# Kernel optimization log

Measured on AMD Instinct MI355X. Metric: run time of the kernel, lower is better.

Reference implementation:

```python
import jax, jax.numpy as jnp
import numpy as np

N, M, KNN, KUP, POS_DIM = 15872, 35637, 5, 20, 32


def _pos_emb_table(n, d):
    # transformer-style sinusoidal table (matches PosEmb._define_pos_emb)
    pos = np.arange(n, dtype=np.float32)[:, None]
    i2 = np.arange(0, d, 2, dtype=np.float32)
    div = 10000.0 ** (i2 / d)
    pe = np.zeros((n, d), dtype=np.float32)
    pe[:, 0::2] = np.sin(pos / div)
    pe[:, 1::2] = np.cos(pos / div)
    return jnp.asarray(pe)


def _lrelu(x):
    return jnp.where(x > 0, x, 0.2 * x)


def _gather(x, idx):
    # x: [B,n,d], idx: [B,m,k] -> [B,m,k,d]
    return jax.vmap(lambda xb, ib: xb[ib])(x, idx)


def _knn_idx(x, k):
    # x: [B,n,d]; k nearest excluding self (torch knn drops column 0 of topk)
    xx = jnp.sum(x * x, axis=-1)
    neg = 2.0 * jnp.einsum('bnd,bmd->bnm', x, x) - xx[:, :, None] - xx[:, None, :]
    _, idx = jax.lax.top_k(neg, k + 1)
    return idx[..., 1:]


def _emb_block(feat, idx, ec_w1, ec_s1, ec_h1, ec_w2, ec_b2,
               w1, s1, h1, w2, s2, h2, w3, s3, h3, w4, b4):
    # get_graph_feature: [B,n,k,2*in] = cat(nbr - ctr, ctr)
    nbr = _gather(feat, idx)
    ctr = jnp.broadcast_to(feat[:, :, None, :], nbr.shape)
    e = jnp.concatenate([nbr - ctr, ctr], axis=-1)
    # edge_conv (1x1 conv2d = per-edge linear); BN folded into scale/shift (eval mode)
    e = _lrelu(jnp.einsum('bnkc,oc->bnko', e, ec_w1) * ec_s1 + ec_h1)
    e = jnp.einsum('bnkc,oc->bnko', e, ec_w2) + ec_b2
    f1 = jnp.max(e, axis=2)                                   # max over k neighbors -> [B,n,out]
    fmax = jnp.broadcast_to(jnp.max(f1, axis=1, keepdims=True), f1.shape)
    favg = jnp.broadcast_to(jnp.mean(f1, axis=1, keepdims=True), f1.shape)
    h = jnp.concatenate([feat, f1, fmax, favg], axis=-1)      # [B,n,3*out+in]
    # fc_out: 1x1 conv1d stack = per-point MLP with folded BN + LeakyReLU
    h = _lrelu(h @ w1.T * s1 + h1)
    h = _lrelu(h @ w2.T * s2 + h2)
    h = _lrelu(h @ w3.T * s3 + h3)
    return h @ w4.T + b4


def _forward(lx, ldx, pos_emb,
             b0_ec_w1, b0_ec_s1, b0_ec_h1, b0_ec_w2, b0_ec_b2,
             b0_fc_w1, b0_fc_s1, b0_fc_h1, b0_fc_w2, b0_fc_s2, b0_fc_h2,
             b0_fc_w3, b0_fc_s3, b0_fc_h3, b0_fc_w4, b0_fc_b4,
             b1_ec_w1, b1_ec_s1, b1_ec_h1, b1_ec_w2, b1_ec_b2,
             b1_fc_w1, b1_fc_s1, b1_fc_h1, b1_fc_w2, b1_fc_s2, b1_fc_h2,
             b1_fc_w3, b1_fc_s3, b1_fc_h3, b1_fc_w4, b1_fc_b4,
             up_inputs, up_w0, up_s0, up_h0, up_w_rest, up_s_rest, up_h_rest, up_wf, up_bf,
             dec_w0, dec_b0, dec_w1, dec_b1, dec_w2, dec_b2, dec_w3, dec_b3,
             dec_w4, dec_b4, dec_wf, dec_bf,
             idx0, up_idx):
    B = ldx.shape[0]
    feat_in = jnp.concatenate([ldx, jnp.broadcast_to(pos_emb[None], (B,) + pos_emb.shape)], axis=-1)  # [B,N,35]
    f0 = _emb_block(feat_in, idx0,
                    b0_ec_w1, b0_ec_s1, b0_ec_h1, b0_ec_w2, b0_ec_b2,
                    b0_fc_w1, b0_fc_s1, b0_fc_h1, b0_fc_w2, b0_fc_s2, b0_fc_h2,
                    b0_fc_w3, b0_fc_s3, b0_fc_h3, b0_fc_w4, b0_fc_b4)   # [B,N,64]
    idx1 = _knn_idx(f0, KNN)                                            # dynamic feature-space KNN
    f1 = _emb_block(f0, idx1,
                    b1_ec_w1, b1_ec_s1, b1_ec_h1, b1_ec_w2, b1_ec_b2,
                    b1_fc_w1, b1_fc_s1, b1_fc_h1, b1_fc_w2, b1_fc_s2, b1_fc_h2,
                    b1_fc_w3, b1_fc_s3, b1_fc_h3, b1_fc_w4, b1_fc_b4)   # [B,N,128]
    x_feat = jnp.concatenate([feat_in, f0, f1], axis=-1)                # [B,N,227]
    # Upscale: SIREN-activated 1x1-conv stack -> softmax interpolation weights over KUP lo-res nbrs
    h = jnp.sin(jnp.einsum('bmkc,oc->bmko', up_inputs[:B], up_w0) * up_s0 + up_h0)
    for i in range(up_w_rest.shape[0]):
        h = jnp.sin(jnp.einsum('bmkc,oc->bmko', h, up_w_rest[i]) * up_s_rest[i] + up_h_rest[i])
    logits = jnp.einsum('bmkc,oc->bmko', h, up_wf) + up_bf              # [B,M,KUP,1]
    w = jax.nn.softmax(logits, axis=2)
    grouped = _gather(x_feat, up_idx)                                   # [B,M,KUP,227]
    z = jnp.sum(w * grouped, axis=2)                                    # [B,M,227]
    # SIREN decoder: dims [227,256,128,64,32,16,3]; zip with 5 mods applies first 5 layers + head
    h = jnp.sin(30.0 * (z @ dec_w0.T + dec_b0))
    h = jnp.sin(h @ dec_w1.T + dec_b1)
    h = jnp.sin(h @ dec_w2.T + dec_b2)
    h = jnp.sin(h @ dec_w3.T + dec_b3)
    h = jnp.sin(h @ dec_w4.T + dec_b4)
    return h @ dec_wf.T + dec_bf                                        # [B,M,3]


def setup_inputs():
    key = jax.random.key(0)
    ks = iter(jax.random.split(key, 100))
    def rn(*s):
        return jax.random.normal(next(ks), s, jnp.float32) * 0.05
    def sc(*s):
        return jax.random.uniform(next(ks), s, jnp.float32, minval=0.5, maxval=1.5)
    inp = {}
    inp['lx'] = jax.random.normal(next(ks), (1, N, 3), jnp.float32)
    inp['ldx'] = jax.random.normal(next(ks), (1, N, 3), jnp.float32)
    inp['pos_emb'] = _pos_emb_table(N, POS_DIM)
    inp['idx0'] = jax.random.randint(next(ks), (1, N, KNN), 0, N - 1)
    # EmbModule 0: in=35, out=64
    inp['b0_ec_w1'], inp['b0_ec_s1'], inp['b0_ec_h1'] = rn(128, 70), sc(128), rn(128)
    inp['b0_ec_w2'], inp['b0_ec_b2'] = rn(64, 128), rn(64)
    inp['b0_fc_w1'], inp['b0_fc_s1'], inp['b0_fc_h1'] = rn(192, 227), sc(192), rn(192)
    inp['b0_fc_w2'], inp['b0_fc_s2'], inp['b0_fc_h2'] = rn(128, 192), sc(128), rn(128)
    inp['b0_fc_w3'], inp['b0_fc_s3'], inp['b0_fc_h3'] = rn(64, 128), sc(64), rn(64)
    inp['b0_fc_w4'], inp['b0_fc_b4'] = rn(64, 64), rn(64)
    # EmbModule 1: in=64, out=128
    inp['b1_ec_w1'], inp['b1_ec_s1'], inp['b1_ec_h1'] = rn(256, 128), sc(256), rn(256)
    inp['b1_ec_w2'], inp['b1_ec_b2'] = rn(128, 256), rn(128)
    inp['b1_fc_w1'], inp['b1_fc_s1'], inp['b1_fc_h1'] = rn(384, 448), sc(384), rn(384)
    inp['b1_fc_w2'], inp['b1_fc_s2'], inp['b1_fc_h2'] = rn(256, 384), sc(256), rn(256)
    inp['b1_fc_w3'], inp['b1_fc_s3'], inp['b1_fc_h3'] = rn(128, 256), sc(128), rn(128)
    inp['b1_fc_w4'], inp['b1_fc_b4'] = rn(128, 128), rn(128)
    inp['up_inputs'] = jax.random.uniform(next(ks), (1, M, KUP, 7), jnp.float32)
    inp['up_idx'] = jax.random.randint(next(ks), (1, M, KUP), 0, N - 1)
    inp['up_w0'], inp['up_s0'], inp['up_h0'] = rn(128, 7), sc(128), rn(128)
    inp['up_w_rest'], inp['up_s_rest'], inp['up_h_rest'] = rn(7, 128, 128), sc(7, 128), rn(7, 128)
    inp['up_wf'], inp['up_bf'] = rn(1, 128), rn(1)
    # SIREN decoder
    dd = [227, 256, 128, 64, 32, 16]
    for i in range(5):
        inp['dec_w%d' % i], inp['dec_b%d' % i] = rn(dd[i + 1], dd[i]), rn(dd[i + 1])
    inp['dec_wf'], inp['dec_bf'] = rn(3, 16), rn(3)
    return inp


def reference(lx, ldx, pos_emb, idx0,
              b0_ec_w1, b0_ec_s1, b0_ec_h1, b0_ec_w2, b0_ec_b2,
              b0_fc_w1, b0_fc_s1, b0_fc_h1, b0_fc_w2, b0_fc_s2, b0_fc_h2,
              b0_fc_w3, b0_fc_s3, b0_fc_h3, b0_fc_w4, b0_fc_b4,
              b1_ec_w1, b1_ec_s1, b1_ec_h1, b1_ec_w2, b1_ec_b2,
              b1_fc_w1, b1_fc_s1, b1_fc_h1, b1_fc_w2, b1_fc_s2, b1_fc_h2,
              b1_fc_w3, b1_fc_s3, b1_fc_h3, b1_fc_w4, b1_fc_b4,
              up_inputs, up_idx, up_w0, up_s0, up_h0,
              up_w_rest, up_s_rest, up_h_rest, up_wf, up_bf,
              dec_w0, dec_b0, dec_w1, dec_b1, dec_w2, dec_b2, dec_w3, dec_b3,
              dec_w4, dec_b4, dec_wf, dec_bf):
    return _forward(lx, ldx, pos_emb,
                    b0_ec_w1, b0_ec_s1, b0_ec_h1, b0_ec_w2, b0_ec_b2,
                    b0_fc_w1, b0_fc_s1, b0_fc_h1, b0_fc_w2, b0_fc_s2, b0_fc_h2,
                    b0_fc_w3, b0_fc_s3, b0_fc_h3, b0_fc_w4, b0_fc_b4,
                    b1_ec_w1, b1_ec_s1, b1_ec_h1, b1_ec_w2, b1_ec_b2,
                    b1_fc_w1, b1_fc_s1, b1_fc_h1, b1_fc_w2, b1_fc_s2, b1_fc_h2,
                    b1_fc_w3, b1_fc_s3, b1_fc_h3, b1_fc_w4, b1_fc_b4,
                    up_inputs, up_w0, up_s0, up_h0, up_w_rest, up_s_rest, up_h_rest, up_wf, up_bf,
                    dec_w0, dec_b0, dec_w1, dec_b1, dec_w2, dec_b2, dec_w3, dec_b3,
                    dec_w4, dec_b4, dec_wf, dec_bf,
                    idx0, up_idx)
```

## Files before the change

### kernel.cpp

```cpp
#include <hip/hip_runtime.h>
#include <hip/hip_bf16.h>
#include <math.h>

#define N_PTS 15872
#define M_PTS 35637
#define KNN_K 5
#define KUP   20
#define UP_ROWS (M_PTS * KUP)
#define NTILE (N_PTS/32)
#define N_EDGE (N_PTS*KNN_K)
#define CDIV(a,b) (((a)+(b)-1)/(b))

typedef __hip_bfloat16 bf16;
typedef unsigned int uint;
typedef unsigned short ushort_t;
__device__ __forceinline__ float b2f(bf16 x){ return __bfloat162float(x); }

__device__ __forceinline__ uint f2bf_bits(float x){
  uint u = __float_as_uint(x);
  return (u + 0x7FFFu + ((u>>16)&1u)) >> 16;
}

__device__ __forceinline__ ushort_t f2h_bits(float x){
  union { _Float16 h; ushort_t u; } c; c.h = (_Float16)x; return c.u;
}

typedef __attribute__((ext_vector_type(8))) short bf16x8;
typedef __attribute__((ext_vector_type(8))) _Float16 f16x8;
typedef __attribute__((ext_vector_type(16))) float f32x16;
union FragAB { bf16x8 v; uint u[4]; };
union FragB  { bf16x8 v; uint4 q; };
union FragH  { f16x8 v; uint4 q; _Float16 h[8]; };
union Acc16  { f32x16 v; float f[16]; };

__global__ void flag_k(const uint* __restrict__ pos_raw, int* __restrict__ flag){
  if (threadIdx.x == 0 && blockIdx.x == 0)
    flag[0] = (pos_raw[0] == 0x3F800000u) ? 1 : 0;
}

struct CvtTab { const void* src[52]; int start[52]; };
__global__ __launch_bounds__(256) void cvt_all_k(CvtTab tab, float* __restrict__ dst,
                                                 const int* __restrict__ flag, int total){
  int i = blockIdx.x*256 + threadIdx.x;
  if (i >= total) return;
  int s = 0;
#pragma unroll 1
  for (int k = 1; k < 52; k++) if (tab.start[k] <= i) s = k;
  int off = i - tab.start[s];
  float v = flag[0] ? b2f(((const bf16*)tab.src[s])[off]) : ((const float*)tab.src[s])[off];
  dst[i] = v;
}

__global__ void packfrag16_k(const float* __restrict__ w, const float* __restrict__ sr,
                             ushort_t* __restrict__ out, int n){
  int i = blockIdx.x*256 + threadIdx.x;
  if (i >= n) return;
  int j = i & 7;
  int lam = (i >> 3) & 63;
  int fg = i >> 9;
  int t = fg & 3, ks = (fg >> 2) & 1, Q = (fg >> 3) & 3, l = fg >> 5;
  int nn = t*32 + (lam & 31);
  int kk = Q*32 + ks*16 + (lam >> 5)*8 + j;
  float x = w[l*16384 + nn*128 + kk] * sr[l*128 + nn];
  out[i] = f2h_bits(x);
}

__global__ void packw_mfma_k(const float* __restrict__ w, ushort_t* __restrict__ whi,
                             ushort_t* __restrict__ wlo, int N, int K, int Kpad, int total){
  int i = blockIdx.x*256 + threadIdx.x;
  if (i >= total) return;
  int j = i & 7;
  int lane = (i >> 3) & 63;
  int fr = i >> 9;
  int nq = Kpad >> 5;
  int ks = fr & 1;
  int q  = (fr >> 1) % nq;
  int nt = (fr >> 1) / nq;
  int n = nt*32 + (lane & 31);
  int k = q*32 + ks*16 + (lane >> 5)*8 + j;
  float x = (n < N && k < K) ? w[(size_t)n*K + k] : 0.f;
  uint hb = f2bf_bits(x);
  uint lb = f2bf_bits(x - __uint_as_float(hb << 16));
  whi[i] = (ushort_t)hb;
  wlo[i] = (ushort_t)lb;
}

__global__ void packknn_k(const float* __restrict__ xf, const float* __restrict__ nr,
                          ushort_t* __restrict__ ahi, ushort_t* __restrict__ alo,
                          ushort_t* __restrict__ bhi, ushort_t* __restrict__ blo){
  int i = blockIdx.x*256 + threadIdx.x;
  if (i >= NTILE*5*64*8) return;
  int e = i & 7;
  int lane = (i >> 3) & 63;
  int rest = i >> 9;
  int kc = rest % 5, jt = rest / 5;
  int n = jt*32 + (lane & 31);
  int k = kc*16 + (lane >> 5)*8 + e;
  float f = (k < 64) ? xf[(size_t)n*227 + 35 + k] : 0.f;
  float av, bv;
  if (k < 64)      { av = 2.f*f;   bv = f; }
  else if (k == 64){ av = nr[n];   bv = -1.f; }
  else if (k == 65){ av = 1.f;     bv = -nr[n]; }
  else             { av = 0.f;     bv = 0.f; }
  uint ah = f2bf_bits(av); uint al = f2bf_bits(av - __uint_as_float(ah<<16));
  uint bh = f2bf_bits(bv); uint bl = f2bf_bits(bv - __uint_as_float(bh<<16));
  ahi[i] = (ushort_t)ah; alo[i] = (ushort_t)al;
  bhi[i] = (ushort_t)bh; blo[i] = (ushort_t)bl;
}

__global__ void fillmark_k(bf16* __restrict__ out, int n){
  int i = blockIdx.x*256 + threadIdx.x;
  if (i < n) out[i] = __float2bfloat16(12345.0f);
}

template<int EPI, int ACT>
__global__ __launch_bounds__(256) void gemm_k(
    const float* __restrict__ A, int lda,
    const float* __restrict__ W, int ldw,
    const float* __restrict__ scale, const float* __restrict__ shift,
    float gmul, float* __restrict__ C, int ldc,
    int M, int Nout, int K)
{
  __shared__ __align__(16) float As[16][64];
  __shared__ __align__(16) float Ws[16][64];
  const int tid = threadIdx.x;
  const int tx = tid & 15, ty = tid >> 4;
  const int bm = blockIdx.x * 64, bn = blockIdx.y * 64;
  const int ar = tid >> 2, ak = (tid & 3) * 4;
  float acc[4][4] = {};
  for (int k0 = 0; k0 < K; k0 += 16) {
    float a0=0.f,a1=0.f,a2=0.f,a3=0.f;
    int grow = bm + ar;
    if (grow < M) {
      const float* ap = A + (size_t)grow * lda + (k0 + ak);
      int rem = K - (k0 + ak);
      if (rem >= 4) { a0=ap[0]; a1=ap[1]; a2=ap[2]; a3=ap[3]; }
      else { if(rem>0)a0=ap[0]; if(rem>1)a1=ap[1]; if(rem>2)a2=ap[2]; }
    }
    float w0=0.f,w1=0.f,w2=0.f,w3=0.f;
    int gn = bn + ar;
    if (gn < Nout) {
      const float* wp = W + (size_t)gn * ldw + (k0 + ak);
      int rem = K - (k0 + ak);
      if (rem >= 4) { w0=wp[0]; w1=wp[1]; w2=wp[2]; w3=wp[3]; }
      else { if(rem>0)w0=wp[0]; if(rem>1)w1=wp[1]; if(rem>2)w2=wp[2]; }
    }
    __syncthreads();
    As[ak+0][ar]=a0; As[ak+1][ar]=a1; As[ak+2][ar]=a2; As[ak+3][ar]=a3;
    Ws[ak+0][ar]=w0; Ws[ak+1][ar]=w1; Ws[ak+2][ar]=w2; Ws[ak+3][ar]=w3;
    __syncthreads();
#pragma unroll
    for (int kk = 0; kk < 16; kk++) {
      float4 av = *reinterpret_cast<const float4*>(&As[kk][ty*4]);
      float4 wv = *reinterpret_cast<const float4*>(&Ws[kk][tx*4]);
      float aa[4] = {av.x,av.y,av.z,av.w};
      float ww[4] = {wv.x,wv.y,wv.z,wv.w};
#pragma unroll
      for (int i=0;i<4;i++)
#pragma unroll
        for (int j=0;j<4;j++) acc[i][j] += aa[i]*ww[j];
    }
  }
#pragma unroll
  for (int i=0;i<4;i++){
    int m = bm + ty*4 + i;
    if (m >= M) continue;
#pragma unroll
    for (int j=0;j<4;j++){
      int n = bn + tx*4 + j;
      if (n >= Nout) continue;
      float v = acc[i][j];
      if (EPI==0)      v = v * scale[n] + shift[n];
      else if (EPI==1) v = v + shift[n];
      else             v = (v + shift[n]) * gmul;
      if (ACT==1)      v = v > 0.f ? v : 0.2f*v;
      else if (ACT==2) v = sinf(v);
      C[(size_t)m*ldc + n] = v;
    }
  }
}

struct MLayer { int K, N, Kq, Nt, woff, soff, hoff, epi, act; float gmul; };
struct MCfg { MLayer L[6]; };

template<int NL, int OUTMODE>
__global__ __launch_bounds__(256) void mlp_fused_k(
    const float* __restrict__ A0, int lda0, int K0, int M,
    MCfg cfg,
    const ushort_t* __restrict__ wh, const ushort_t* __restrict__ wl,
    const float* __restrict__ wc,
    float* __restrict__ Cout, int ldc,
    void* __restrict__ oflg, const int* __restrict__ flag)
{
  __shared__ __align__(16) uint slab[64*256];
  const int tid = threadIdx.x;
  const int lane = tid & 63;
  const int wv = tid >> 6;
  const int np = lane & 31;
  const int hb2 = lane >> 5;
  const int rhalf = wv & 1, thalf = wv >> 1;
  const int rb = blockIdx.x * 64;
  const int row_l = rhalf*32 + np;

  for (int e = tid; e < 64*64; e += 256) {
    int r = e >> 6, g = e & 63;
    int gr = rb + r;
    uint p[4];
#pragma unroll
    for (int u=0;u<4;u++){
      int k = g*4+u;
      float f = (gr < M && k < K0) ? A0[(size_t)gr*lda0 + k] : 0.f;
      uint hb = f2bf_bits(f);
      uint lb = f2bf_bits(f - __uint_as_float(hb<<16));
      p[u] = (hb<<16) | lb;
    }
    *(uint4*)&slab[r*256 + (((g ^ r) & 63)<<2)] = make_uint4(p[0],p[1],p[2],p[3]);
  }
  __syncthreads();

#pragma unroll 1
  for (int l = 0; l < NL; l++){
    const int N = cfg.L[l].N, Kq = cfg.L[l].Kq, Nt = cfg.L[l].Nt;
    const int woff = cfg.L[l].woff, soff = cfg.L[l].soff, hoff = cfg.L[l].hoff;
    const int epi = cfg.L[l].epi, actf = cfg.L[l].act;
    const float gmul = cfg.L[l].gmul;
    Acc16 acc[4];
#pragma unroll
    for (int u=0;u<4;u++)
#pragma unroll
      for (int i=0;i<16;i++) acc[u].f[i] = 0.f;

#pragma unroll 1
    for (int q = 0; q < Kq; q++){
#pragma unroll
      for (int ks = 0; ks < 2; ks++){
        int g0 = (q*32 + ks*16 + hb2*8) >> 2;
        uint4 a0 = *(const uint4*)&slab[row_l*256 + ((((g0  ) ^ row_l) & 63)<<2)];
        uint4 a1 = *(const uint4*)&slab[row_l*256 + ((((g0+1) ^ row_l) & 63)<<2)];
        uint au[8] = {a0.x,a0.y,a0.z,a0.w,a1.x,a1.y,a1.z,a1.w};
        FragAB ah, al;
#pragma unroll
        for (int p=0;p<4;p++){
          ah.u[p] = (au[2*p]>>16)     | (au[2*p+1] & 0xFFFF0000u);
          al.u[p] = (au[2*p]&0xFFFFu) | (au[2*p+1]<<16);
        }
#pragma unroll
        for (int u=0;u<4;u++){
          int t = thalf + u*2;
          if (t < Nt){
            size_t fb = (size_t)woff + ((size_t)((t*Kq + q)*2 + ks))*512 + (size_t)lane*8;
            FragB bh, bl;
            bh.q = *(const uint4*)(wh + fb);
            bl.q = *(const uint4*)(wl + fb);
            acc[u].v = __builtin_amdgcn_mfma_f32_32x32x16_bf16(ah.v, bh.v, acc[u].v, 0,0,0);
            acc[u].v = __builtin_amdgcn_mfma_f32_32x32x16_bf16(al.v, bh.v, acc[u].v, 0,0,0);
            acc[u].v = __builtin_amdgcn_mfma_f32_32x32x16_bf16(ah.v, bl.v, acc[u].v, 0,0,0);
          }
        }
      }
    }
    __syncthreads();
#pragma unroll
    for (int u=0;u<4;u++){
      int t = thalf + u*2;
      if (t < Nt){
        int col = t*32 + np;
        if (col < N){
          float scv = (epi==0) ? wc[soff+col] : 0.f;
          float shv = wc[hoff+col];
#pragma unroll
          for (int reg=0;reg<16;reg++){
            int r32 = (reg&3) + 8*(reg>>2) + 4*hb2;
            float v = acc[u].f[reg];
            if (epi==0)      v = v*scv + shv;
            else if (epi==1) v = v + shv;
            else             v = (v + shv)*gmul;
            if (actf==1)      v = v > 0.f ? v : 0.2f*v;
            else if (actf==2) v = __sinf(v);
            if (l == NL-1){
              int gr = rb + rhalf*32 + r32;
              if (gr < M){
                if (OUTMODE==0) Cout[(size_t)gr*ldc + col] = v;
                else {
                  if (!(fabsf(v) < 1e30f)) v = 777.0f;
                  size_t oi = (size_t)gr*3 + col;
                  if (flag[0]) ((bf16*)oflg)[oi] = __float2bfloat16(v);
                  else         ((float*)oflg)[oi] = v;
                }
              }
            } else {
              int r = rhalf*32 + r32;
              uint hb = f2bf_bits(v);
              uint lb = f2bf_bits(v - __uint_as_float(hb<<16));
              slab[r*256 + ((((col>>2) ^ r) & 63)<<2) + (col&3)] = (hb<<16) | lb;
            }
          }
        }
      }
    }
    __syncthreads();
  }
}

#define INS5(tv, tj, v, j) \
  if ((v) > tv[4]){ tv[4]=(v); tj[4]=(j); \
    _Pragma("unroll") \
    for (int q=4;q>0;q--) \
      if (tv[q] > tv[q-1]){ float tf=tv[q-1]; tv[q-1]=tv[q]; tv[q]=tf; \
                            int ti=tj[q-1]; tj[q-1]=tj[q]; tj[q]=ti; } }

__global__ __launch_bounds__(256) void knn_mfma_k(
    const ushort_t* __restrict__ ahi, const ushort_t* __restrict__ alo,
    const ushort_t* __restrict__ bhi, const ushort_t* __restrict__ blo,
    int* __restrict__ out)
{
  __shared__ float mv[4][32][5];
  __shared__ int   mjj[4][32][5];
  const int tid = threadIdx.x;
  const int lane = tid & 63;
  const int wv = tid >> 6;
  const int np = lane & 31;
  const int hb2 = lane >> 5;
  const int it = blockIdx.x;
  const int ig = it*32 + np;

  FragB vh[5], vl[5];
  {
    size_t bb = (size_t)(it*5)*512 + (size_t)lane*8;
#pragma unroll
    for (int kc=0;kc<5;kc++){
      vh[kc].q = *(const uint4*)(bhi + bb + kc*512);
      vl[kc].q = *(const uint4*)(blo + bb + kc*512);
    }
  }

  float tv[5] = {-1e30f,-1e30f,-1e30f,-1e30f,-1e30f};
  int   tj[5] = {0,0,0,0,0};

  FragB uh[5], ul[5], nh[5], nl[5];
  {
    size_t ab = (size_t)(wv*5)*512 + (size_t)lane*8;
#pragma unroll
    for (int kc=0;kc<5;kc++){
      uh[kc].q = *(const uint4*)(ahi + ab + kc*512);
      ul[kc].q = *(const uint4*)(alo + ab + kc*512);
    }
  }

#pragma unroll 1
  for (int t = 0; t < NTILE/4; t++){
    int jt = wv + t*4;
    if (t+1 < NTILE/4){
      size_t an = (size_t)((jt+4)*5)*512 + (size_t)lane*8;
#pragma unroll
      for (int kc=0;kc<5;kc++){
        nh[kc].q = *(const uint4*)(ahi + an + kc*512);
        nl[kc].q = *(const uint4*)(alo + an + kc*512);
      }
    }
    Acc16 acc;
#pragma unroll
    for (int q=0;q<16;q++) acc.f[q] = 0.f;
#pragma unroll
    for (int kc=0;kc<5;kc++){
      acc.v = __builtin_amdgcn_mfma_f32_32x32x16_bf16(uh[kc].v, vh[kc].v, acc.v, 0,0,0);
      acc.v = __builtin_amdgcn_mfma_f32_32x32x16_bf16(ul[kc].v, vh[kc].v, acc.v, 0,0,0);
      acc.v = __builtin_amdgcn_mfma_f32_32x32x16_bf16(uh[kc].v, vl[kc].v, acc.v, 0,0,0);
    }
    int jb = jt*32 + 4*hb2;
#pragma unroll
    for (int reg=0;reg<16;reg++){
      int j = jb + (reg&3) + 8*(reg>>2);
      float v = acc.f[reg];
      if (j != ig) { INS5(tv, tj, v, j); }
    }
    if (t+1 < NTILE/4){
#pragma unroll
      for (int kc=0;kc<5;kc++){ uh[kc] = nh[kc]; ul[kc] = nl[kc]; }
    }
  }

#pragma unroll
  for (int s=0;s<5;s++){
    float ov = __shfl_xor(tv[s], 32, 64);
    int   oj = __shfl_xor(tj[s], 32, 64);
    INS5(tv, tj, ov, oj);
  }
  if (hb2 == 0){
#pragma unroll
    for (int s=0;s<5;s++){ mv[wv][np][s] = tv[s]; mjj[wv][np][s] = tj[s]; }
  }
  __syncthreads();
  if (tid < 32){
    float bv[5]; int bj[5];
#pragma unroll
    for (int s=0;s<5;s++){ bv[s] = mv[0][tid][s]; bj[s] = mjj[0][tid][s]; }
#pragma unroll
    for (int w=1;w<4;w++)
#pragma unroll
      for (int s=0;s<5;s++){
        float v = mv[w][tid][s]; int j = mjj[w][tid][s];
        INS5(bv, bj, v, j);
      }
    int gi = it*32 + tid;
#pragma unroll
    for (int s=0;s<5;s++) out[gi*KNN_K + s] = bj[s];
  }
}

__global__ __launch_bounds__(256, 3) void siren_fused_k(
    const void* __restrict__ upin,
    const ushort_t* __restrict__ wf16,
    const float* __restrict__ W0c, const float* __restrict__ S0c, const float* __restrict__ H0c,
    const float* __restrict__ HRc,
    const float* __restrict__ WFc, const float* __restrict__ BFc,
    float* __restrict__ logits, const int* __restrict__ flag)
{
  __shared__ __align__(16) ushort_t act[4*32*128];
  __shared__ float intile[4*32*8];
  __shared__ float w0s[128*9];
  __shared__ float wfs[128];
  __shared__ float bfs[1];

  const int tid  = threadIdx.x;
  const int lane = tid & 63;
  const int wv   = tid >> 6;
  const int np   = lane & 31;
  const int hb2  = lane >> 5;
  const int rowbase = blockIdx.x * 128 + wv * 32;
  const int isbf = flag[0];
  ushort_t* actw = act + wv*32*128;
  float* intw = intile + wv*32*8;

  for (int e = tid; e < 128*7; e += 256) w0s[(e/7)*9 + (e%7)] = W0c[e];
  if (tid < 128) wfs[tid] = WFc[tid];
  if (tid == 0) bfs[0] = BFc[0];
  for (int e = lane; e < 32*7; e += 64) {
    int r = e/7, k = e%7;
    int gr = rowbase + r;
    float v = 0.f;
    if (gr < UP_ROWS)
      v = isbf ? b2f(((const bf16*)upin)[(size_t)gr*7+k]) : ((const float*)upin)[(size_t)gr*7+k];
    intw[r*8+k] = v;
  }
  __syncthreads();

#pragma unroll
  for (int t = 0; t < 4; t++) {
    int c = t*32 + np;
    float s = S0c[c], b = H0c[c];
    int gc = c >> 3;
    int co = np & 7;
#pragma unroll
    for (int reg = 0; reg < 16; reg++) {
      int r = (reg&3) + 8*(reg>>2) + 4*hb2;
      float a = 0.f;
#pragma unroll
      for (int k = 0; k < 7; k++) a += intw[r*8+k]*w0s[c*9+k];
      float x = __sinf(a*s + b);
      actw[r*128 + (((gc ^ (r & 15)) << 3) | co)] = f2h_bits(x);
    }
  }

#pragma unroll 1
  for (int l = 0; l < 7; l++) {
    float sh[4];
#pragma unroll
    for (int t=0;t<4;t++) sh[t] = HRc[l*128 + t*32 + np];
    Acc16 acc[4];
#pragma unroll
    for (int t=0;t<4;t++)
#pragma unroll
      for (int i=0;i<16;i++) acc[t].f[i] = 0.f;

#pragma unroll 1
    for (int Q = 0; Q < 4; Q++) {
#pragma unroll
      for (int ks = 0; ks < 2; ks++) {
        int g = Q*4 + ks*2 + hb2;
        FragH af;
        af.q = *(const uint4*)&actw[np*128 + ((g ^ (np & 15)) << 3)];
        size_t fb = ((size_t)(((l*4 + Q)*2 + ks)*4) << 9) + (size_t)lane*8;
        FragH bh[4];
#pragma unroll
        for (int t=0;t<4;t++)
          bh[t].q = *(const uint4*)(wf16 + fb + (size_t)t*512);
#pragma unroll
        for (int t=0;t<4;t++)
          acc[t].v = __builtin_amdgcn_mfma_f32_32x32x16_f16(af.v, bh[t].v, acc[t].v, 0,0,0);
      }
    }
#pragma unroll
    for (int t=0;t<4;t++){
      int c = t*32 + np;
      int gc = c >> 3;
      int co = np & 7;
#pragma unroll
      for (int reg=0;reg<16;reg++){
        int r = (reg&3) + 8*(reg>>2) + 4*hb2;
        float x = __sinf(acc[t].f[reg] + sh[t]);
        actw[r*128 + (((gc ^ (r & 15)) << 3) | co)] = f2h_bits(x);
      }
    }
  }

  {
    float a = 0.f;
#pragma unroll
    for (int g = 0; g < 8; g++) {
      int gg = hb2*8 + g;
      FragH u;
      u.q = *(const uint4*)&actw[np*128 + ((gg ^ (np & 15)) << 3)];
      int kb = gg*8;
#pragma unroll
      for (int e = 0; e < 8; e++) a += (float)u.h[e] * wfs[kb+e];
    }
    a += __shfl_xor(a, 32, 64);
    int gr = rowbase + np;
    if (hb2 == 0 && gr < UP_ROWS) logits[gr] = a + bfs[0];
  }
}

__global__ void featin_k(const void* __restrict__ ldx, const void* __restrict__ pos,
                         float* __restrict__ xf, const int* __restrict__ flag){
  int i = blockIdx.x*256 + threadIdx.x;
  if (i >= N_PTS*35) return;
  int n = i / 35, c = i % 35;
  float v;
  if (flag[0]) {
    v = (c < 3) ? b2f(((const bf16*)ldx)[n*3+c]) : b2f(((const bf16*)pos)[n*32 + (c-3)]);
  } else {
    v = (c < 3) ? ((const float*)ldx)[n*3+c] : ((const float*)pos)[n*32 + (c-3)];
  }
  xf[(size_t)n*227 + c] = v;
}

__global__ void gather_e_k(const float* __restrict__ xf, int coff, int CIN,
                           const int* __restrict__ idx, float* __restrict__ e,
                           int n0, int np){
  int W2 = 2*CIN;
  int i = blockIdx.x*256 + threadIdx.x;
  if (i >= np*KNN_K*W2) return;
  int c = i % W2; int ek = i / W2;
  int nl = ek / KNN_K, k = ek % KNN_K;
  int n = n0 + nl;
  int j = idx[n*KNN_K + k];
  float out;
  if (c < CIN) out = xf[(size_t)j*227 + coff + c] - xf[(size_t)n*227 + coff + c];
  else         out = xf[(size_t)n*227 + coff + (c-CIN)];
  e[(size_t)ek*W2 + c] = out;
}

__global__ void kmax_k(const float* __restrict__ e2, int C, float* __restrict__ f1,
                       int n0, int np){
  int i = blockIdx.x*256 + threadIdx.x;
  if (i >= np*C) return;
  int nl = i / C, c = i % C;
  float v = -1e30f;
  for (int k=0;k<KNN_K;k++) v = fmaxf(v, e2[((size_t)nl*KNN_K+k)*C + c]);
  f1[(size_t)(n0+nl)*C + c] = v;
}

template<int C>
__global__ __launch_bounds__(256) void reduce1_k(const float* __restrict__ X, int n,
                                                 float* __restrict__ pmax, float* __restrict__ psum){
  const int tid = threadIdx.x;
  const int c = tid % C;
  const int r0 = tid / C;
  const int TPR = 256 / C;
  float vmax = -1e30f, vsum = 0.f;
  for (int row = blockIdx.x * TPR + r0; row < n; row += gridDim.x * TPR) {
    float v = X[(size_t)row * C + c];
    vmax = fmaxf(vmax, v); vsum += v;
  }
  __shared__ float smax[256], ssum[256];
  smax[tid]=vmax; ssum[tid]=vsum;
  __syncthreads();
  if (tid < C) {
    for (int q=1;q<TPR;q++){ vmax=fmaxf(vmax, smax[q*C+c]); vsum += ssum[q*C+c]; }
    pmax[blockIdx.x*C + c] = vmax; psum[blockIdx.x*C + c] = vsum;
  }
}

template<int C>
__global__ void reduce2_k(const float* __restrict__ pmax, const float* __restrict__ psum,
                          int nblk, float invn, float* __restrict__ fmaxo, float* __restrict__ favgo){
  int c = threadIdx.x; if (c >= C) return;
  float vmax=-1e30f, vsum=0.f;
  for (int b=0;b<nblk;b++){ vmax=fmaxf(vmax,pmax[b*C+c]); vsum+=psum[b*C+c]; }
  fmaxo[c]=vmax; favgo[c]=vsum*invn;
}

__global__ void concat_k(const float* __restrict__ xf, int coff, int CF,
                         const float* __restrict__ f1, int C,
                         const float* __restrict__ fmax, const float* __restrict__ favg,
                         float* __restrict__ h, int n0, int np){
  int W = CF + 3*C;
  int i = blockIdx.x*256 + threadIdx.x;
  if (i >= np*W) return;
  int nl = i / W, c = i % W;
  int n = n0 + nl;
  float v;
  if (c < CF)          v = xf[(size_t)n*227 + coff + c];
  else if (c < CF+C)   v = f1[(size_t)n*C + (c-CF)];
  else if (c < CF+2*C) v = fmax[c-CF-C];
  else                 v = favg[c-CF-2*C];
  h[(size_t)nl*W + c] = v;
}

__global__ void norms_k(const float* __restrict__ xf, float* __restrict__ nr){
  int n = blockIdx.x*256 + threadIdx.x;
  if (n >= N_PTS) return;
  const float* p = xf + (size_t)n*227 + 35;
  float s = 0.f;
  for (int d=0;d<64;d++) s += p[d]*p[d];
  nr[n] = s;
}

__global__ __launch_bounds__(64) void softgather_k(const float* __restrict__ logits,
                                                   const int* __restrict__ up_idx,
                                                   const float* __restrict__ xf,
                                                   float* __restrict__ z){
  __shared__ float lw[KUP]; __shared__ int li[KUP];
  int m = blockIdx.x;
  int tid = threadIdx.x;
  if (tid < KUP){ lw[tid] = logits[(size_t)m*KUP + tid]; li[tid] = up_idx[(size_t)m*KUP + tid]; }
  __syncthreads();
  float mx = -1e30f;
  for (int k=0;k<KUP;k++) mx = fmaxf(mx, lw[k]);
  __syncthreads();
  if (tid < KUP) lw[tid] = expf(lw[tid]-mx);
  __syncthreads();
  float s = 0.f;
  for (int k=0;k<KUP;k++) s += lw[k];
  float inv = 1.f/s;
  for (int c = tid; c < 227; c += 64){
    float acc = 0.f;
    for (int k=0;k<KUP;k++) acc += lw[k] * xf[(size_t)li[k]*227 + c];
    z[(size_t)m*227 + c] = acc*inv;
  }
}

extern "C" void kernel_launch(void* const* d_in, const int* in_sizes, int n_in,
                              void* d_out, int out_size, void* d_ws, size_t ws_size,
                              hipStream_t stream) {
  const int *idx0  = (const int*)d_in[3];
  const int *upidx = (const int*)d_in[37];

  float* ws = (float*)d_ws;
  float* x_feat = ws;
  float* f1b    = ws + 3602944;
  float* pmax   = ws + 5634560;
  float* psum   = ws + 5667328;
  float* fmaxv  = ws + 5700096;
  float* favgv  = ws + 5700224;
  int*   flag   = (int*)(ws + 5700352);
  int*   idx1   = (int*)(ws + 5700368);
  float* nrm    = ws + 5779728;
  float* logits = ws + 5795600;
  float* wcvt   = ws + 6508352;
  float* S      = ws + 7214400;
  ushort_t* whi  = (ushort_t*)(S + 9662464);
  ushort_t* wlo  = whi + 114688;
  ushort_t* gwhi = wlo + 114688;
  ushort_t* gwlo = gwhi + 331776;

  const size_t NEED = (size_t)(7214400 + 9662464) * 4
                    + (size_t)(114688*2 + 331776*2) * 2;
  if (ws_size < NEED) {
    fillmark_k<<<CDIV(out_size,256),256,0,stream>>>((bf16*)d_out, out_size);
    return;
  }

  flag_k<<<1,64,0,stream>>>((const uint*)d_in[2], flag);
  CvtTab tab;
  int wcoff = 0, seg = 0;
  auto CVT = [&](int i, int n)->const float* {
    tab.src[seg] = d_in[i]; tab.start[seg] = wcoff; seg++;
    const float* p = wcvt + wcoff; wcoff += n;
    return p;
  };
  const float *E0W1=CVT(4,8960),  *E0S1=CVT(5,128),  *E0H1=CVT(6,128),
              *E0W2=CVT(7,8192),  *E0B2=CVT(8,64);
  const float *F0W1=CVT(9,43584), *F0S1=CVT(10,192), *F0H1=CVT(11,192),
              *F0W2=CVT(12,24576),*F0S2=CVT(13,128), *F0H2=CVT(14,128),
              *F0W3=CVT(15,8192), *F0S3=CVT(16,64),  *F0H3=CVT(17,64),
              *F0W4=CVT(18,4096), *F0B4=CVT(19,64);
  const float *E1W1=CVT(20,32768),*E1S1=CVT(21,256), *E1H1=CVT(22,256),
              *E1W2=CVT(23,32768),*E1B2=CVT(24,128);
  const float *F1W1=CVT(25,172032),*F1S1=CVT(26,384),*F1H1=CVT(27,384),
              *F1W2=CVT(28,98304),*F1S2=CVT(29,256), *F1H2=CVT(30,256),
              *F1W3=CVT(31,32768),*F1S3=CVT(32,128), *F1H3=CVT(33,128),
              *F1W4=CVT(34,16384),*F1B4=CVT(35,128);
  const float *UPW0=CVT(38,896),  *UPS0=CVT(39,128), *UPH0=CVT(40,128),
              *UPWR=CVT(41,114688),*UPSR=CVT(42,896),*UPHR=CVT(43,896),
              *UPWF=CVT(44,128),  *UPBF=CVT(45,1);
  const float *DW0=CVT(46,58112), *DB0=CVT(47,256),
              *DW1=CVT(48,32768), *DB1=CVT(49,128),
              *DW2=CVT(50,8192),  *DB2=CVT(51,64),
              *DW3=CVT(52,2048),  *DB3=CVT(53,32),
              *DW4=CVT(54,512),   *DB4=CVT(55,16),
              *DWF=CVT(56,48),    *DBF=CVT(57,3);
  cvt_all_k<<<CDIV(wcoff,256),256,0,stream>>>(tab, wcvt, flag, wcoff);

  packfrag16_k<<<CDIV(114688,256),256,0,stream>>>(UPWR, UPSR, whi, 114688);

  int offs[16]; const float* srcs[16]; int Ns[16], Ks[16], Kps[16];
  {
    int o = 0, q = 0;
    auto REG = [&](const float* s, int N, int K, int Kpad){
      srcs[q]=s; Ns[q]=N; Ks[q]=K; Kps[q]=Kpad; offs[q]=o;
      o += CDIV(N,32)*32*Kpad; q++;
    };
    REG(F0W1,192,227,256); REG(F0W2,128,192,192); REG(F0W3,64,128,128); REG(F0W4,64,64,64);
    REG(DW0,256,227,256);  REG(DW1,128,256,256);  REG(DW2,64,128,128);
    REG(DW3,32,64,64);     REG(DW4,16,32,32);     REG(DWF,3,16,32);
    REG(E0W1,128,70,96);   REG(E0W2,64,128,128);
    REG(E1W1,256,128,128); REG(E1W2,128,256,256);
    REG(F1W3,128,256,256); REG(F1W4,128,128,128);
  }
  for (int q = 0; q < 16; q++){
    int total = CDIV(Ns[q],32)*32*Kps[q];
    packw_mfma_k<<<CDIV(total,256),256,0,stream>>>(srcs[q], gwhi+offs[q], gwlo+offs[q],
                                                   Ns[q], Ks[q], Kps[q], total);
  }

  auto OFF = [&](const float* p){ return (int)(p - wcvt); };
  MCfg cfc0{};
  cfc0.L[0] = {227,192,8,6, offs[0], OFF(F0S1), OFF(F0H1), 0,1, 0.f};
  cfc0.L[1] = {192,128,6,4, offs[1], OFF(F0S2), OFF(F0H2), 0,1, 0.f};
  cfc0.L[2] = {128, 64,4,2, offs[2], OFF(F0S3), OFF(F0H3), 0,1, 0.f};
  cfc0.L[3] = { 64, 64,2,2, offs[3], 0,         OFF(F0B4), 1,0, 0.f};
  MCfg cdec{};
  cdec.L[0] = {227,256,8,8, offs[4], 0, OFF(DB0), 2,2, 30.f};
  cdec.L[1] = {256,128,8,4, offs[5], 0, OFF(DB1), 1,2, 0.f};
  cdec.L[2] = {128, 64,4,2, offs[6], 0, OFF(DB2), 1,2, 0.f};
  cdec.L[3] = { 64, 32,2,1, offs[7], 0, OFF(DB3), 1,2, 0.f};
  cdec.L[4] = { 32, 16,1,1, offs[8], 0, OFF(DB4), 1,2, 0.f};
  cdec.L[5] = { 16,  3,1,1, offs[9], 0, OFF(DBF), 1,0, 0.f};
  MCfg ce0{};
  ce0.L[0] = { 70,128,3,4, offs[10], OFF(E0S1), OFF(E0H1), 0,1, 0.f};
  ce0.L[1] = {128, 64,4,2, offs[11], 0,         OFF(E0B2), 1,0, 0.f};
  MCfg ce1{};
  ce1.L[0] = {128,256,4,8, offs[12], OFF(E1S1), OFF(E1H1), 0,1, 0.f};
  ce1.L[1] = {256,128,8,4, offs[13], 0,         OFF(E1B2), 1,0, 0.f};
  MCfg cf1t{};
  cf1t.L[0] = {256,128,8,4, offs[14], OFF(F1S3), OFF(F1H3), 0,1, 0.f};
  cf1t.L[1] = {128,128,4,4, offs[15], 0,         OFF(F1B4), 1,0, 0.f};

  const float invN = 1.f/(float)N_PTS;
  const int CHN = 8192;

  featin_k<<<CDIV(N_PTS*35,256),256,0,stream>>>(d_in[1], d_in[2], x_feat, flag);

  {
    const int P0 = N_PTS/2;
    for (int n0 = 0; n0 < N_PTS; n0 += P0) {
      int ne = P0 * KNN_K;
      float* eA   = S;
      float* eOut = S + 2777600;
      gather_e_k<<<CDIV(ne*70,256),256,0,stream>>>(x_feat, 0, 35, idx0, eA, n0, P0);
      mlp_fused_k<2,0><<<CDIV(ne,64),256,0,stream>>>(
          eA,70,70,ne, ce0, gwhi,gwlo,wcvt, eOut,64, nullptr, flag);
      kmax_k<<<CDIV(P0*64,256),256,0,stream>>>(eOut, 64, f1b, n0, P0);
    }
  }
  reduce1_k<64><<<256,256,0,stream>>>(f1b, N_PTS, pmax, psum);
  reduce2_k<64><<<1,64,0,stream>>>(pmax, psum, 256, invN, fmaxv, favgv);
  {
    float* h = S;
    concat_k<<<CDIV(N_PTS*227,256),256,0,stream>>>(x_feat,0,35, f1b,64, fmaxv,favgv, h, 0, N_PTS);
    mlp_fused_k<4,0><<<CDIV(N_PTS,64),256,0,stream>>>(
        h,227,227,N_PTS, cfc0, gwhi,gwlo,wcvt, x_feat+35,227, nullptr, flag);
  }

  norms_k<<<CDIV(N_PTS,256),256,0,stream>>>(x_feat, nrm);
  {
    const int PLANE = NTILE*5*64*8;
    ushort_t* ajhi = (ushort_t*)S;
    ushort_t* ajlo = ajhi + PLANE;
    ushort_t* bihi = ajlo + PLANE;
    ushort_t* bilo = bihi + PLANE;
    packknn_k<<<CDIV(PLANE,256),256,0,stream>>>(x_feat, nrm, ajhi, ajlo, bihi, bilo);
    knn_mfma_k<<<NTILE,256,0,stream>>>(ajhi, ajlo, bihi, bilo, idx1);
  }

  {
    const int P1 = 5952;
    for (int n0 = 0; n0 < N_PTS; n0 += P1) {
      int np = N_PTS - n0; if (np > P1) np = P1;
      int ne = np * KNN_K;
      float* eA   = S;
      float* eOut = S + 3809280;
      gather_e_k<<<CDIV(ne*128,256),256,0,stream>>>(x_feat, 35, 64, idx1, eA, n0, np);
      mlp_fused_k<2,0><<<CDIV(ne,64),256,0,stream>>>(
          eA,128,128,ne, ce1, gwhi,gwlo,wcvt, eOut,128, nullptr, flag);
      kmax_k<<<CDIV(np*128,256),256,0,stream>>>(eOut, 128, f1b, n0, np);
    }
  }
  reduce1_k<128><<<256,256,0,stream>>>(f1b, N_PTS, pmax, psum);
  reduce2_k<128><<<1,128,0,stream>>>(pmax, psum, 256, invN, fmaxv, favgv);
  for (int n0 = 0; n0 < N_PTS; n0 += CHN) {
    int np = N_PTS - n0; if (np > CHN) np = CHN;
    float* h  = S;
    float* a1 = S + 3670016;
    int gx = CDIV(np,64);
    concat_k<<<CDIV(np*448,256),256,0,stream>>>(x_feat,35,64, f1b,128, fmaxv,favgv, h, n0, np);
    gemm_k<0,1><<<dim3(gx,6),256,0,stream>>>(h,448,  F1W1,448, F1S1,F1H1,0.f, a1,384, np,384,448);
    gemm_k<0,1><<<dim3(gx,4),256,0,stream>>>(a1,384, F1W2,384, F1S2,F1H2,0.f, h,256,  np,256,384);
    mlp_fused_k<2,0><<<gx,256,0,stream>>>(
        h,256,256,np, cf1t, gwhi,gwlo,wcvt, x_feat+(size_t)n0*227+99,227, nullptr, flag);
  }

  siren_fused_k<<<CDIV(UP_ROWS,128),256,0,stream>>>(
      d_in[36], whi, UPW0, UPS0, UPH0, UPHR, UPWF, UPBF, logits, flag);
  float* zbuf = S;
  softgather_k<<<M_PTS,64,0,stream>>>(logits, upidx, x_feat, zbuf);

  mlp_fused_k<6,1><<<CDIV(M_PTS,64),256,0,stream>>>(
      zbuf,227,227,M_PTS, cdec, gwhi,gwlo,wcvt, nullptr,0, d_out, flag);
}
```

Baseline: 2.013 ms.

## Swap MFMA operand order so SIREN activations store as packed row vectors

Swaps the A/B operands of the SIREN MFMA so each lane's accumulator holds consecutive output channels of one row. This lets the sine outputs be packed with cvt_pkrtz and written to LDS as 8-byte vectors instead of scalar 2-byte stores. The first layer folds the scale and shift into padded shared weights and writes 16-byte packed chunks, and the per-layer shifts are preloaded into LDS. The occupancy hint in launch_bounds is dropped, and the rounding mode changes from round-to-nearest to round-toward-zero fp16.

```diff
diff --git a/kernel.cpp b/kernel.cpp
--- a/kernel.cpp
+++ b/kernel.cpp
@@ -27,11 +27,13 @@
 
 typedef __attribute__((ext_vector_type(8))) short bf16x8;
 typedef __attribute__((ext_vector_type(8))) _Float16 f16x8;
+typedef __attribute__((ext_vector_type(2))) __fp16 fp16x2_t;
 typedef __attribute__((ext_vector_type(16))) float f32x16;
 union FragAB { bf16x8 v; uint u[4]; };
 union FragB  { bf16x8 v; uint4 q; };
 union FragH  { f16x8 v; uint4 q; _Float16 h[8]; };
 union Acc16  { f32x16 v; float f[16]; };
+union H2U    { fp16x2_t h; uint u; };
 
 __global__ void flag_k(const uint* __restrict__ pos_raw, int* __restrict__ flag){
   if (threadIdx.x == 0 && blockIdx.x == 0)
@@ -408,7 +410,7 @@
   }
 }
 
-__global__ __launch_bounds__(256, 3) void siren_fused_k(
+__global__ __launch_bounds__(256) void siren_fused_k(
     const void* __restrict__ upin,
     const ushort_t* __restrict__ wf16,
     const float* __restrict__ W0c, const float* __restrict__ S0c, const float* __restrict__ H0c,
@@ -418,7 +420,8 @@
 {
   __shared__ __align__(16) ushort_t act[4*32*128];
   __shared__ float intile[4*32*8];
-  __shared__ float w0s[128*9];
+  __shared__ __align__(16) float w0s[128*8];
+  __shared__ __align__(16) float hrs[7*128];
   __shared__ float wfs[128];
   __shared__ float bfs[1];
 
@@ -427,12 +430,19 @@
   const int wv   = tid >> 6;
   const int np   = lane & 31;
   const int hb2  = lane >> 5;
+  const int npx  = np & 15;
   const int rowbase = blockIdx.x * 128 + wv * 32;
   const int isbf = flag[0];
   ushort_t* actw = act + wv*32*128;
   float* intw = intile + wv*32*8;
-
-  for (int e = tid; e < 128*7; e += 256) w0s[(e/7)*9 + (e%7)] = W0c[e];
+  const int abase = np*128;
+
+  for (int e = tid; e < 128*7; e += 256){
+    int c = e/7, k = e%7;
+    w0s[c*8+k] = W0c[e]*S0c[c];
+  }
+  if (tid < 128) w0s[tid*8+7] = H0c[tid];
+  for (int e = tid; e < 7*128; e += 256) hrs[e] = HRc[e];
   if (tid < 128) wfs[tid] = WFc[tid];
   if (tid == 0) bfs[0] = BFc[0];
   for (int e = lane; e < 32*7; e += 64) {
@@ -445,28 +455,35 @@
   }
   __syncthreads();
 
-#pragma unroll
-  for (int t = 0; t < 4; t++) {
-    int c = t*32 + np;
-    float s = S0c[c], b = H0c[c];
-    int gc = c >> 3;
-    int co = np & 7;
-#pragma unroll
-    for (int reg = 0; reg < 16; reg++) {
-      int r = (reg&3) + 8*(reg>>2) + 4*hb2;
-      float a = 0.f;
-#pragma unroll
-      for (int k = 0; k < 7; k++) a += intw[r*8+k]*w0s[c*9+k];
-      float x = __sinf(a*s + b);
-      actw[r*128 + (((gc ^ (r & 15)) << 3) | co)] = f2h_bits(x);
+  {
+    float xin[7];
+#pragma unroll
+    for (int k=0;k<7;k++) xin[k] = intw[np*8+k];
+#pragma unroll
+    for (int gg = 0; gg < 8; gg++) {
+      int g = hb2*8 + gg;
+      float x[8];
+#pragma unroll
+      for (int j=0;j<8;j++){
+        int c = g*8 + j;
+        const float4 wa = *(const float4*)&w0s[c*8];
+        const float4 wb = *(const float4*)&w0s[c*8+4];
+        float a = wb.w;
+        a += xin[0]*wa.x; a += xin[1]*wa.y; a += xin[2]*wa.z; a += xin[3]*wa.w;
+        a += xin[4]*wb.x; a += xin[5]*wb.y; a += xin[6]*wb.z;
+        x[j] = __sinf(a);
+      }
+      H2U c0,c1,c2,c3;
+      c0.h = __builtin_amdgcn_cvt_pkrtz(x[0],x[1]);
+      c1.h = __builtin_amdgcn_cvt_pkrtz(x[2],x[3]);
+      c2.h = __builtin_amdgcn_cvt_pkrtz(x[4],x[5]);
+      c3.h = __builtin_amdgcn_cvt_pkrtz(x[6],x[7]);
+      *(uint4*)&actw[abase + ((g ^ npx)<<3)] = make_uint4(c0.u,c1.u,c2.u,c3.u);
     }
   }
 
 #pragma unroll 1
   for (int l = 0; l < 7; l++) {
-    float sh[4];
-#pragma unroll
-    for (int t=0;t<4;t++) sh[t] = HRc[l*128 + t*32 + np];
     Acc16 acc[4];
 #pragma unroll
     for (int t=0;t<4;t++)
@@ -479,27 +496,30 @@
       for (int ks = 0; ks < 2; ks++) {
         int g = Q*4 + ks*2 + hb2;
         FragH af;
-        af.q = *(const uint4*)&actw[np*128 + ((g ^ (np & 15)) << 3)];
-        size_t fb = ((size_t)(((l*4 + Q)*2 + ks)*4) << 9) + (size_t)lane*8;
-        FragH bh[4];
-#pragma unroll
-        for (int t=0;t<4;t++)
-          bh[t].q = *(const uint4*)(wf16 + fb + (size_t)t*512);
-#pragma unroll
-        for (int t=0;t<4;t++)
-          acc[t].v = __builtin_amdgcn_mfma_f32_32x32x16_f16(af.v, bh[t].v, acc[t].v, 0,0,0);
+        af.q = *(const uint4*)&actw[abase + ((g ^ npx) << 3)];
+        int fb = (((l*4 + Q)*2 + ks)*4 << 9) + lane*8;
+#pragma unroll
+        for (int t=0;t<4;t++){
+          FragH bh;
+          bh.q = *(const uint4*)(wf16 + fb + t*512);
+          acc[t].v = __builtin_amdgcn_mfma_f32_32x32x16_f16(bh.v, af.v, acc[t].v, 0,0,0);
+        }
       }
     }
 #pragma unroll
     for (int t=0;t<4;t++){
-      int c = t*32 + np;
-      int gc = c >> 3;
-      int co = np & 7;
-#pragma unroll
-      for (int reg=0;reg<16;reg++){
-        int r = (reg&3) + 8*(reg>>2) + 4*hb2;
-        float x = __sinf(acc[t].f[reg] + sh[t]);
-        actw[r*128 + (((gc ^ (r & 15)) << 3) | co)] = f2h_bits(x);
+#pragma unroll
+      for (int rg=0;rg<4;rg++){
+        int g = t*4 + rg;
+        const float4 bb = *(const float4*)&hrs[l*128 + g*8 + 4*hb2];
+        float x0 = __sinf(acc[t].f[rg*4+0] + bb.x);
+        float x1 = __sinf(acc[t].f[rg*4+1] + bb.y);
+        float x2 = __sinf(acc[t].f[rg*4+2] + bb.z);
+        float x3 = __sinf(acc[t].f[rg*4+3] + bb.w);
+        H2U u0,u1;
+        u0.h = __builtin_amdgcn_cvt_pkrtz(x0,x1);
+        u1.h = __builtin_amdgcn_cvt_pkrtz(x2,x3);
+        *(uint2*)&actw[abase + ((g ^ npx)<<3) + 4*hb2] = make_uint2(u0.u,u1.u);
       }
     }
   }
@@ -510,7 +530,7 @@
     for (int g = 0; g < 8; g++) {
       int gg = hb2*8 + g;
       FragH u;
-      u.q = *(const uint4*)&actw[np*128 + ((gg ^ (np & 15)) << 3)];
+      u.q = *(const uint4*)&actw[abase + ((gg ^ npx) << 3)];
       int kb = gg*8;
 #pragma unroll
       for (int e = 0; e < 8; e++) a += (float)u.h[e] * wfs[kb+e];
```

Measured after the change: 2.052 ms. Within noise of the previous version (+1.9%).
